# Kernel tuning notes

Hardware: AMD Instinct MI355X
Metric: run time of the kernel (lower is better)

Reference implementation:

```python
import jax, jax.numpy as jnp
import numpy as np

B, T, C_IN, C_HID, C_EMB, K, MAX_DUR = 16, 512, 512, 256, 384, 5, 8
MAX_MEL = T * MAX_DUR  # static upper bound on regulated length (4096)
LRELU_SLOPE = 0.3
PAD = (K - 1) // 2
EPS = 1e-5


def setup_inputs() -> dict:
    key = jax.random.key(0)
    ks = jax.random.split(key, 14)
    s = 0.05
    return {
        "x": jax.random.normal(ks[0], (B, T, C_IN), jnp.float32),
        "x_res": jax.random.normal(ks[1], (B, T, C_IN), jnp.float32),
        "duration_target": jax.random.randint(ks[2], (B, T), 0, MAX_DUR, dtype=jnp.int32),
        "embeddings": jax.random.normal(ks[3], (B, T, C_EMB), jnp.float32),
        "src_mask": jnp.zeros((B, T), jnp.bool_),
        "conv1_w": s * jax.random.normal(ks[4], (K, C_IN, C_HID), jnp.float32),
        "conv1_b": jnp.zeros((C_HID,), jnp.float32),
        "ln1_g": jnp.ones((C_HID,), jnp.float32),
        "ln1_b": jnp.zeros((C_HID,), jnp.float32),
        "conv2_w": s * jax.random.normal(ks[5], (K, C_HID, C_HID), jnp.float32),
        "conv2_b": jnp.zeros((C_HID,), jnp.float32),
        "ln2_g": jnp.ones((C_HID,), jnp.float32),
        "ln2_b": jnp.zeros((C_HID,), jnp.float32),
        "lin_w": s * jax.random.normal(ks[6], (C_HID, 1), jnp.float32),
        "lin_b": jnp.zeros((1,), jnp.float32),
    }


def _conv1d(x, w, b):
    # x: [B, T, Cin], w: [K, Cin, Cout] -> [B, T, Cout] (same padding)
    y = jax.lax.conv_general_dilated(
        x, w, window_strides=(1,), padding=[(PAD, PAD)],
        dimension_numbers=("NWC", "WIO", "NWC"))
    return y + b


def _layer_norm(x, g, b):
    mu = jnp.mean(x, axis=-1, keepdims=True)
    var = jnp.mean(jnp.square(x - mu), axis=-1, keepdims=True)
    return (x - mu) * jax.lax.rsqrt(var + EPS) * g + b


def _duration_predictor(x, mask, c1w, c1b, g1, b1, c2w, c2b, g2, b2, lw, lb):
    h = jax.nn.leaky_relu(_conv1d(x, c1w, c1b), LRELU_SLOPE)
    h = _layer_norm(h, g1, b1)  # dropout is identity at eval
    h = jax.nn.leaky_relu(_conv1d(h, c2w, c2b), LRELU_SLOPE)
    h = _layer_norm(h, g2, b2)
    h = (h @ lw + lb).squeeze(-1)  # [B, T]
    return jnp.where(mask, 0.0, h)


def _length_regulate(x, duration):
    # Fused prefix-sum + gather replacement for the looped expand/cat/pad.
    # token i occupies output frames [cumsum[i-1], cumsum[i])
    cum = jnp.cumsum(duration, axis=1)              # [B, T]
    total = cum[:, -1]                              # [B] mel lengths
    pos = jnp.arange(MAX_MEL, dtype=cum.dtype)      # [MAX_MEL]
    idx = jax.vmap(lambda c: jnp.searchsorted(c, pos, side="right"))(cum)  # [B, MAX_MEL]
    idx = jnp.clip(idx, 0, duration.shape[1] - 1)
    valid = (pos[None, :] < total[:, None])         # [B, MAX_MEL]
    out = jnp.take_along_axis(x, idx[..., None], axis=1)
    out = out * valid[..., None].astype(x.dtype)    # zero-padded past mel_len
    return out, total.astype(jnp.int32)


def reference(x, x_res, duration_target, embeddings, src_mask,
              conv1_w, conv1_b, ln1_g, ln1_b, conv2_w, conv2_b, ln2_g, ln2_b,
              lin_w, lin_b):
    # upsample_train path: x_res is detached before the duration predictor
    x_res = jax.lax.stop_gradient(x_res)
    log_duration_prediction = _duration_predictor(
        x_res, src_mask, conv1_w, conv1_b, ln1_g, ln1_b,
        conv2_w, conv2_b, ln2_g, ln2_b, lin_w, lin_b)
    x_up, _ = _length_regulate(x, duration_target)
    emb_up, _ = _length_regulate(embeddings, duration_target)
    return x_up, log_duration_prediction, emb_up
```

## Files before the change

kernel.cpp:

```cpp
#include <hip/hip_runtime.h>


constexpr int Bn = 16, Tn = 512, CIN1 = 512, CHID = 256, CEMB = 384, MAXMEL = 4096;
constexpr int NROWS = Bn * Tn;
#define LRELU 0.3f
#define EPSV 1e-5f

typedef __attribute__((ext_vector_type(8))) short bf16x8;
typedef __attribute__((ext_vector_type(4))) float f32x4;
typedef __attribute__((ext_vector_type(16))) float f32x16;
typedef __attribute__((ext_vector_type(4))) unsigned int u32x4;
typedef unsigned short ushort_t;

static __device__ __forceinline__ ushort_t f2bf(float f) {
  unsigned u = __builtin_bit_cast(unsigned, f);
  unsigned r = (u + 0x7fffu + ((u >> 16) & 1u)) >> 16;
  return (ushort_t)r;
}

__global__ __launch_bounds__(256) void wprep_kernel(const float* __restrict__ w1src,
                                                    const float* __restrict__ w2src,
                                                    ushort_t* __restrict__ w1dst,
                                                    ushort_t* __restrict__ w2dst) {
  const int blk = blockIdx.x;
  const float* src;
  ushort_t* dst;
  int CI, fr0, sh;
  if (blk < 320) { src = w1src; dst = w1dst; CI = 512; sh = 5; fr0 = blk * 4; }
  else           { src = w2src; dst = w2dst; CI = 256; sh = 4; fr0 = (blk - 320) * 4; }
  const int wv = threadIdx.x >> 6, l = threadIdx.x & 63;
  const int fr = fr0 + wv;
  const int cob32 = fr & 7;
  const int t = fr >> 3;
  const int ksh = t >> sh;
  const int ci16 = t & ((1 << sh) - 1);
  const int ci = ci16 * 16 + (l >> 5) * 8;
  const int co = cob32 * 32 + (l & 31);
  ushort_t v[8];
#pragma unroll
  for (int j = 0; j < 8; ++j)
    v[j] = f2bf(src[((size_t)(ksh * CI + ci + j)) * 256 + co]);
  u32x4 pack;
#pragma unroll
  for (int q = 0; q < 4; ++q)
    pack[q] = (unsigned)v[q * 2] | ((unsigned)v[q * 2 + 1] << 16);
  *(u32x4*)&dst[(size_t)fr * 512 + l * 8] = pack;
}

template <int CI, bool F32IN>
__global__ __launch_bounds__(256, 2) void conv_mfma_kernel(
    const float* __restrict__ xin,
    const ushort_t* __restrict__ inbf,
    const ushort_t* __restrict__ wB,
    float* __restrict__ hraw) {
  constexpr int NCHUNK = CI / 128;
  constexpr int ROWS = 36, LDSTRIDE = 136;
  __shared__ ushort_t sA[ROWS * LDSTRIDE];

  const int mt = blockIdx.x, ns = blockIdx.y;
  const int b = mt >> 4, t0 = (mt & 15) * 32;
  const int tid = threadIdx.x;
  const int l = tid & 63, nh = tid >> 6;
  const int lm = l & 31, lq = l >> 5;
  const int cob32 = ns * 4 + nh;

  f32x16 acc;
#pragma unroll
  for (int i = 0; i < 16; ++i) acc[i] = 0.f;

  const ushort_t* pB = wB + (size_t)cob32 * 512 + l * 8;

#pragma unroll 1
  for (int chunk = 0; chunk < NCHUNK; ++chunk) {
    {
      const int cibase = chunk * 128;
#pragma unroll 1
      for (int i = 0; i < 9; ++i) {
        const int p = i * 256 + tid;
        const int r = p >> 6, c2 = (p & 63) * 2;
        const int t = t0 - 2 + r;
        unsigned hv = 0;
        if ((unsigned)t < (unsigned)Tn) {
          const size_t src = (size_t)(b * Tn + t) * CI + cibase + c2;
          if (F32IN) {
            const float2 v = *(const float2*)(xin + src);
            hv = (unsigned)f2bf(v.x) | ((unsigned)f2bf(v.y) << 16);
          } else {
            hv = *(const unsigned*)(inbf + src);
          }
        }
        const int sw = ((r >> 3) & 3) << 3;
        *(unsigned*)&sA[r * LDSTRIDE + (c2 ^ sw)] = hv;
      }
    }
    __syncthreads();

#pragma unroll 1
    for (int ksh = 0; ksh < 5; ++ksh) {
      const int r = lm + ksh;
      const int sw = ((r >> 3) & 3) << 3;
      const size_t bbase = (size_t)((ksh * (CI / 16) + chunk * 8) * 8) * 512;
#pragma unroll
      for (int kk = 0; kk < 8; ++kk) {
        const int c = (kk * 16 + lq * 8) ^ sw;
        const bf16x8 a = *(const bf16x8*)&sA[r * LDSTRIDE + c];
        const bf16x8 bv = *(const bf16x8*)(pB + bbase + (size_t)kk * 8 * 512);
        acc = __builtin_amdgcn_mfma_f32_32x32x16_bf16(a, bv, acc, 0, 0, 0);
      }
    }
    __syncthreads();
  }

  const int col = ns * 128 + nh * 32 + lm;
  float* pOut = hraw + (size_t)(b * Tn + t0) * 256 + col;
#pragma unroll
  for (int reg = 0; reg < 16; ++reg) {
    const int row = (reg & 3) + 8 * (reg >> 2) + 4 * lq;
    pOut[(size_t)row * 256] = acc[reg];
  }
}

template <bool FINAL>
__global__ __launch_bounds__(256) void ln_kernel(
    const float* __restrict__ hraw,
    const float* __restrict__ bias, const float* __restrict__ g,
    const float* __restrict__ be, ushort_t* __restrict__ h1,
    const float* __restrict__ lw, const float* __restrict__ lb,
    const unsigned char* __restrict__ mask, float* __restrict__ ldp) {
  const int row = blockIdx.x * 4 + (threadIdx.x >> 6);
  const int l = threadIdx.x & 63;
  const f32x4 p = ((const f32x4*)hraw)[row * 64 + l];
  const f32x4 bi = ((const f32x4*)bias)[l];
  float v0 = p.x + bi.x, v1 = p.y + bi.y, v2 = p.z + bi.z, v3 = p.w + bi.w;
  v0 = (v0 > 0.f) ? v0 : LRELU * v0;
  v1 = (v1 > 0.f) ? v1 : LRELU * v1;
  v2 = (v2 > 0.f) ? v2 : LRELU * v2;
  v3 = (v3 > 0.f) ? v3 : LRELU * v3;
  float s = v0 + v1 + v2 + v3;
  float s2 = v0 * v0 + v1 * v1 + v2 * v2 + v3 * v3;
#pragma unroll
  for (int off = 32; off >= 1; off >>= 1) {
    s += __shfl_xor(s, off);
    s2 += __shfl_xor(s2, off);
  }
  const float mu = s * (1.f / 256.f);
  const float var = s2 * (1.f / 256.f) - mu * mu;
  const float rs = rsqrtf(var + EPSV);
  const f32x4 gg = ((const f32x4*)g)[l];
  const f32x4 bb = ((const f32x4*)be)[l];
  const float h0 = (v0 - mu) * rs * gg.x + bb.x;
  const float h1v = (v1 - mu) * rs * gg.y + bb.y;
  const float h2 = (v2 - mu) * rs * gg.z + bb.z;
  const float h3 = (v3 - mu) * rs * gg.w + bb.w;
  if (!FINAL) {
    ushort4 uh;
    uh.x = f2bf(h0); uh.y = f2bf(h1v); uh.z = f2bf(h2); uh.w = f2bf(h3);
    ((ushort4*)h1)[row * 64 + l] = uh;
  } else {
    const f32x4 lv = ((const f32x4*)lw)[l];
    float d = h0 * lv.x + h1v * lv.y + h2 * lv.z + h3 * lv.w;
#pragma unroll
    for (int off = 32; off >= 1; off >>= 1) d += __shfl_xor(d, off);
    if (l == 0) {
      float val = d + lb[0];
      if (mask[row]) val = 0.f;
      ldp[row] = val;
    }
  }
}

__global__ __launch_bounds__(512) void build_idx_kernel(const int* __restrict__ dur,
                                                        int* __restrict__ idx) {
  __shared__ int wsum[8];
  const int b = blockIdx.x, tid = threadIdx.x;
  const int lane = tid & 63, wv = tid >> 6;
  const int d = dur[b * Tn + tid];
  int v = d;
#pragma unroll
  for (int off = 1; off <= 32; off <<= 1) {
    const int t = __shfl_up(v, off);
    if (lane >= off) v += t;
  }
  if (lane == 63) wsum[wv] = v;
  __syncthreads();
  int woff = 0, total = 0;
#pragma unroll
  for (int i = 0; i < 8; ++i) {
    const int s = wsum[i];
    if (i < wv) woff += s;
    total += s;
  }
  const int end = v + woff;
  for (int p = end - d; p < end; ++p) idx[b * MAXMEL + p] = tid;
  for (int p = total + tid; p < MAXMEL; p += 512) idx[b * MAXMEL + p] = -1;
}

__global__ __launch_bounds__(256) void gather_kernel(const float* __restrict__ x,
                                                     const float* __restrict__ emb,
                                                     const int* __restrict__ idx,
                                                     float* __restrict__ x_up,
                                                     float* __restrict__ emb_up) {
  const f32x4* x4 = (const f32x4*)x;
  const f32x4* e4 = (const f32x4*)emb;
  f32x4* xu4 = (f32x4*)x_up;
  f32x4* eu4 = (f32x4*)emb_up;
  const int tid0 = blockIdx.x * 256 + threadIdx.x;
  const int stride = gridDim.x * 256;
  const f32x4 z = (f32x4){0.f, 0.f, 0.f, 0.f};
  for (int u = tid0; u < Bn * MAXMEL * 128; u += stride) {
    const int bp = u >> 7, i = u & 127;
    const int t = idx[bp];
    const int b = bp >> 12;
    const f32x4 v = (t >= 0) ? x4[((b << 9) + t) * 128 + i] : z;
    __builtin_nontemporal_store(v, &xu4[u]);
  }
  for (int u = tid0; u < Bn * MAXMEL * 96; u += stride) {
    const int bp = u / 96, i = u - bp * 96;
    const int t = idx[bp];
    const int b = bp >> 12;
    const f32x4 v = (t >= 0) ? e4[((b << 9) + t) * 96 + i] : z;
    __builtin_nontemporal_store(v, &eu4[u]);
  }
}

extern "C" void kernel_launch(void* const* d_in, const int* in_sizes, int n_in,
                              void* d_out, int out_size, void* d_ws, size_t ws_size,
                              hipStream_t stream) {
  const float* x     = (const float*)d_in[0];
  const float* x_res = (const float*)d_in[1];
  const int*   dur   = (const int*)d_in[2];
  const float* emb   = (const float*)d_in[3];
  const unsigned char* mask = (const unsigned char*)d_in[4];
  const float* c1w = (const float*)d_in[5];
  const float* c1b = (const float*)d_in[6];
  const float* g1  = (const float*)d_in[7];
  const float* b1  = (const float*)d_in[8];
  const float* c2w = (const float*)d_in[9];
  const float* c2b = (const float*)d_in[10];
  const float* g2  = (const float*)d_in[11];
  const float* b2  = (const float*)d_in[12];
  const float* lw  = (const float*)d_in[13];
  const float* lb  = (const float*)d_in[14];

  float* x_up   = (float*)d_out;
  float* ldp    = x_up + (size_t)Bn * MAXMEL * CIN1;
  float* emb_up = ldp + (size_t)Bn * Tn;

  int* idx = (int*)d_ws;
  ushort_t* h1 = (ushort_t*)((char*)d_ws + (size_t)Bn * MAXMEL * 4);
  ushort_t* w1 = h1 + (size_t)NROWS * 256;
  ushort_t* w2 = w1 + (size_t)5 * 512 * 256;
  float* hraw = (float*)(w2 + (size_t)5 * 256 * 256);

  wprep_kernel<<<480, 256, 0, stream>>>(c1w, c2w, w1, w2);
  build_idx_kernel<<<Bn, 512, 0, stream>>>(dur, idx);
  conv_mfma_kernel<512, true><<<dim3(256, 2), 256, 0, stream>>>(
      x_res, nullptr, w1, hraw);
  ln_kernel<false><<<NROWS / 4, 256, 0, stream>>>(
      hraw, c1b, g1, b1, h1, nullptr, nullptr, nullptr, nullptr);
  conv_mfma_kernel<256, false><<<dim3(256, 2), 256, 0, stream>>>(
      nullptr, h1, w2, hraw);
  ln_kernel<true><<<NROWS / 4, 256, 0, stream>>>(
      hraw, c2b, g2, b2, nullptr, lw, lb, mask, ldp);
  gather_kernel<<<2048, 256, 0, stream>>>(x, emb, idx, x_up, emb_up);
}
```

Baseline: 359.7 us.

## Fuse weight prep with index build, co-schedule conv1 with gather

Merges weight bf16 conversion and the duration prefix-sum/index build into one launch. The memory-bound gather now runs as extra blocks of the conv1 launch, so the compute-bound conv1 MFMA work and the bandwidth-bound gather share the GPU at the same time. This cuts two launches and removes the serial tail where the gather ran alone. The risk is that gather blocks contend with conv blocks for bandwidth and occupancy, because both use the same launch bounds and LDS allocation.

```diff
diff --git a/kernel.cpp b/kernel.cpp
--- a/kernel.cpp
+++ b/kernel.cpp
@@ -18,46 +18,15 @@
   return (ushort_t)r;
 }
 
-__global__ __launch_bounds__(256) void wprep_kernel(const float* __restrict__ w1src,
-                                                    const float* __restrict__ w2src,
-                                                    ushort_t* __restrict__ w1dst,
-                                                    ushort_t* __restrict__ w2dst) {
-  const int blk = blockIdx.x;
-  const float* src;
-  ushort_t* dst;
-  int CI, fr0, sh;
-  if (blk < 320) { src = w1src; dst = w1dst; CI = 512; sh = 5; fr0 = blk * 4; }
-  else           { src = w2src; dst = w2dst; CI = 256; sh = 4; fr0 = (blk - 320) * 4; }
-  const int wv = threadIdx.x >> 6, l = threadIdx.x & 63;
-  const int fr = fr0 + wv;
-  const int cob32 = fr & 7;
-  const int t = fr >> 3;
-  const int ksh = t >> sh;
-  const int ci16 = t & ((1 << sh) - 1);
-  const int ci = ci16 * 16 + (l >> 5) * 8;
-  const int co = cob32 * 32 + (l & 31);
-  ushort_t v[8];
-#pragma unroll
-  for (int j = 0; j < 8; ++j)
-    v[j] = f2bf(src[((size_t)(ksh * CI + ci + j)) * 256 + co]);
-  u32x4 pack;
-#pragma unroll
-  for (int q = 0; q < 4; ++q)
-    pack[q] = (unsigned)v[q * 2] | ((unsigned)v[q * 2 + 1] << 16);
-  *(u32x4*)&dst[(size_t)fr * 512 + l * 8] = pack;
-}
-
 template <int CI, bool F32IN>
-__global__ __launch_bounds__(256, 2) void conv_mfma_kernel(
-    const float* __restrict__ xin,
-    const ushort_t* __restrict__ inbf,
-    const ushort_t* __restrict__ wB,
-    float* __restrict__ hraw) {
+static __device__ __forceinline__ void conv_body(
+    int mt, int ns,
+    const float* __restrict__ xin, const ushort_t* __restrict__ inbf,
+    const ushort_t* __restrict__ wB, float* __restrict__ hraw) {
   constexpr int NCHUNK = CI / 128;
   constexpr int ROWS = 36, LDSTRIDE = 136;
   __shared__ ushort_t sA[ROWS * LDSTRIDE];
 
-  const int mt = blockIdx.x, ns = blockIdx.y;
   const int b = mt >> 4, t0 = (mt & 15) * 32;
   const int tid = threadIdx.x;
   const int l = tid & 63, nh = tid >> 6;
@@ -120,6 +89,47 @@
   }
 }
 
+__global__ __launch_bounds__(256, 2) void conv1_gather_kernel(
+    const float* __restrict__ x_res, const ushort_t* __restrict__ w1,
+    float* __restrict__ hraw,
+    const float* __restrict__ x, const float* __restrict__ emb,
+    const int* __restrict__ idx,
+    float* __restrict__ x_up, float* __restrict__ emb_up) {
+  const int blk = blockIdx.x;
+  if (blk < 512) {
+    conv_body<512, true>(blk & 255, blk >> 8, x_res, nullptr, w1, hraw);
+    return;
+  }
+  const f32x4* x4 = (const f32x4*)x;
+  const f32x4* e4 = (const f32x4*)emb;
+  f32x4* xu4 = (f32x4*)x_up;
+  f32x4* eu4 = (f32x4*)emb_up;
+  const int tid0 = (blk - 512) * 256 + threadIdx.x;
+  const int stride = 2048 * 256;
+  const f32x4 z = (f32x4){0.f, 0.f, 0.f, 0.f};
+  for (int u = tid0; u < Bn * MAXMEL * 128; u += stride) {
+    const int bp = u >> 7, i = u & 127;
+    const int t = idx[bp];
+    const int b = bp >> 12;
+    const f32x4 v = (t >= 0) ? x4[((b << 9) + t) * 128 + i] : z;
+    __builtin_nontemporal_store(v, &xu4[u]);
+  }
+  for (int u = tid0; u < Bn * MAXMEL * 96; u += stride) {
+    const int bp = u / 96, i = u - bp * 96;
+    const int t = idx[bp];
+    const int b = bp >> 12;
+    const f32x4 v = (t >= 0) ? e4[((b << 9) + t) * 96 + i] : z;
+    __builtin_nontemporal_store(v, &eu4[u]);
+  }
+}
+
+__global__ __launch_bounds__(256, 2) void conv2_kernel(
+    const ushort_t* __restrict__ h1, const ushort_t* __restrict__ w2,
+    float* __restrict__ hraw) {
+  const int blk = blockIdx.x;
+  conv_body<256, false>(blk & 255, blk >> 8, nullptr, h1, w2, hraw);
+}
+
 template <bool FINAL>
 __global__ __launch_bounds__(256) void ln_kernel(
     const float* __restrict__ hraw,
@@ -169,10 +179,38 @@
   }
 }
 
-__global__ __launch_bounds__(512) void build_idx_kernel(const int* __restrict__ dur,
-                                                        int* __restrict__ idx) {
+__global__ __launch_bounds__(512) void prep_kernel(
+    const float* __restrict__ w1src, const float* __restrict__ w2src,
+    ushort_t* __restrict__ w1dst, ushort_t* __restrict__ w2dst,
+    const int* __restrict__ dur, int* __restrict__ idx) {
   __shared__ int wsum[8];
-  const int b = blockIdx.x, tid = threadIdx.x;
+  const int blk = blockIdx.x;
+  const int tid = threadIdx.x;
+  if (blk < 240) {
+    const float* src;
+    ushort_t* dst;
+    int CI, fr, sh;
+    const int wv = tid >> 6, l = tid & 63;
+    if (blk < 160) { src = w1src; dst = w1dst; CI = 512; sh = 5; fr = blk * 8 + wv; }
+    else           { src = w2src; dst = w2dst; CI = 256; sh = 4; fr = (blk - 160) * 8 + wv; }
+    const int cob32 = fr & 7;
+    const int t = fr >> 3;
+    const int ksh = t >> sh;
+    const int ci16 = t & ((1 << sh) - 1);
+    const int ci = ci16 * 16 + (l >> 5) * 8;
+    const int co = cob32 * 32 + (l & 31);
+    ushort_t v[8];
+#pragma unroll
+    for (int j = 0; j < 8; ++j)
+      v[j] = f2bf(src[((size_t)(ksh * CI + ci + j)) * 256 + co]);
+    u32x4 pack;
+#pragma unroll
+    for (int q = 0; q < 4; ++q)
+      pack[q] = (unsigned)v[q * 2] | ((unsigned)v[q * 2 + 1] << 16);
+    *(u32x4*)&dst[(size_t)fr * 512 + l * 8] = pack;
+    return;
+  }
+  const int b = blk - 240;
   const int lane = tid & 63, wv = tid >> 6;
   const int d = dur[b * Tn + tid];
   int v = d;
@@ -193,34 +231,6 @@
   const int end = v + woff;
   for (int p = end - d; p < end; ++p) idx[b * MAXMEL + p] = tid;
   for (int p = total + tid; p < MAXMEL; p += 512) idx[b * MAXMEL + p] = -1;
-}
-
-__global__ __launch_bounds__(256) void gather_kernel(const float* __restrict__ x,
-                                                     const float* __restrict__ emb,
-                                                     const int* __restrict__ idx,
-                                                     float* __restrict__ x_up,
-                                                     float* __restrict__ emb_up) {
-  const f32x4* x4 = (const f32x4*)x;
-  const f32x4* e4 = (const f32x4*)emb;
-  f32x4* xu4 = (f32x4*)x_up;
-  f32x4* eu4 = (f32x4*)emb_up;
-  const int tid0 = blockIdx.x * 256 + threadIdx.x;
-  const int stride = gridDim.x * 256;
-  const f32x4 z = (f32x4){0.f, 0.f, 0.f, 0.f};
-  for (int u = tid0; u < Bn * MAXMEL * 128; u += stride) {
-    const int bp = u >> 7, i = u & 127;
-    const int t = idx[bp];
-    const int b = bp >> 12;
-    const f32x4 v = (t >= 0) ? x4[((b << 9) + t) * 128 + i] : z;
-    __builtin_nontemporal_store(v, &xu4[u]);
-  }
-  for (int u = tid0; u < Bn * MAXMEL * 96; u += stride) {
-    const int bp = u / 96, i = u - bp * 96;
-    const int t = idx[bp];
-    const int b = bp >> 12;
-    const f32x4 v = (t >= 0) ? e4[((b << 9) + t) * 96 + i] : z;
-    __builtin_nontemporal_store(v, &eu4[u]);
-  }
 }
 
 extern "C" void kernel_launch(void* const* d_in, const int* in_sizes, int n_in,
@@ -252,15 +262,12 @@
   ushort_t* w2 = w1 + (size_t)5 * 512 * 256;
   float* hraw = (float*)(w2 + (size_t)5 * 256 * 256);
 
-  wprep_kernel<<<480, 256, 0, stream>>>(c1w, c2w, w1, w2);
-  build_idx_kernel<<<Bn, 512, 0, stream>>>(dur, idx);
-  conv_mfma_kernel<512, true><<<dim3(256, 2), 256, 0, stream>>>(
-      x_res, nullptr, w1, hraw);
+  prep_kernel<<<256, 512, 0, stream>>>(c1w, c2w, w1, w2, dur, idx);
+  conv1_gather_kernel<<<2560, 256, 0, stream>>>(
+      x_res, w1, hraw, x, emb, idx, x_up, emb_up);
   ln_kernel<false><<<NROWS / 4, 256, 0, stream>>>(
       hraw, c1b, g1, b1, h1, nullptr, nullptr, nullptr, nullptr);
-  conv_mfma_kernel<256, false><<<dim3(256, 2), 256, 0, stream>>>(
-      nullptr, h1, w2, hraw);
+  conv2_kernel<<<512, 256, 0, stream>>>(h1, w2, hraw);
   ln_kernel<true><<<NROWS / 4, 256, 0, stream>>>(
       hraw, c2b, g2, b2, nullptr, lw, lb, mask, ldp);
-  gather_kernel<<<2048, 256, 0, stream>>>(x, emb, idx, x_up, emb_up);
-}
+}
```

Measured after the change: 353.1 us. Within noise of the previous version (-1.8%).
